# Kernel tuning notes

Hardware: AMD Instinct MI355X
Metric: run time of the kernel (lower is better)

## Reference

```python
import jax, jax.numpy as jnp
import numpy as np

N_HEAD = 8
LINEAR_DIM = 64
IN_PIXELS = 4096  # h*w = 64*64
D = N_HEAD * LINEAR_DIM  # 512
C = 128
LN_EPS = 1e-6
BN_EPS = 1e-5


def setup_inputs() -> dict:
    key = jax.random.key(0)
    ks = jax.random.split(key, 10)
    shp = (16, C, 64, 64)
    # Kaiming-uniform-ish small init for weights (torch Linear weight layout: [out, in])
    def lin(k, out_f, in_f):
        lim = 1.0 / np.sqrt(in_f)
        return jax.random.uniform(k, (out_f, in_f), jnp.float32, -lim, lim)
    return {
        "v": jax.random.normal(ks[0], shp, jnp.float32),
        "k": jax.random.normal(ks[1], shp, jnp.float32),
        "q": jax.random.normal(ks[2], shp, jnp.float32),
        "w_qs": lin(ks[3], D, IN_PIXELS),
        "w_ks": lin(ks[4], D, IN_PIXELS),
        "w_vs": lin(ks[5], D, IN_PIXELS),
        "w_fc": lin(ks[6], IN_PIXELS, D),
        "ln_gamma": jnp.ones((D,), jnp.float32),
        "ln_beta": jnp.zeros((D,), jnp.float32),
        "temperature": jnp.asarray(IN_PIXELS ** 0.5, jnp.float32),
        "bn_gamma": jnp.ones((C,), jnp.float32),
        "bn_beta": jnp.zeros((C,), jnp.float32),
    }


def _layer_norm(x, gamma, beta):
    # torch-faithful: unbiased std (ddof=1), divide by (std + eps)
    mean = jnp.mean(x, axis=-1, keepdims=True)
    var = jnp.var(x, axis=-1, keepdims=True, ddof=1)
    std = jnp.sqrt(var)
    return gamma * (x - mean) / (std + LN_EPS) + beta


def reference(v, k, q, w_qs, w_ks, w_vs, w_fc, ln_gamma, ln_beta, temperature, bn_gamma, bn_beta):
    b, c, h, w = q.shape
    P = h * w
    qf = q.reshape(b, c, P)
    kf = k.reshape(b, c, P)
    vf = v.reshape(b, c, P)
    residual = vf
    # QKV projections: [b,c,P] @ W^T -> [b,c,D] -> [b,nh,c,ld]
    def proj(x, W):
        y = jnp.einsum('bcp,dp->bcd', x, W)
        return y.reshape(b, c, N_HEAD, LINEAR_DIM).transpose(0, 2, 1, 3)
    Q = proj(qf, w_qs)
    K = proj(kf, w_ks)
    V = proj(vf, w_vs)
    # channel-wise attention: scores [b,nh,c,c]
    scores = jnp.einsum('bhcd,bhed->bhce', Q / temperature, K)
    attn = jax.nn.softmax(scores, axis=-1)
    O = jnp.einsum('bhce,bhed->bhcd', attn, V)
    O = O.transpose(0, 2, 1, 3).reshape(b, c, N_HEAD * LINEAR_DIM)
    # Swish -> LayerNorm -> fc -> residual
    O = O * jax.nn.sigmoid(O)
    O = _layer_norm(O, ln_gamma, ln_beta)
    O = jnp.einsum('bcd,pd->bcp', O, w_fc)
    out = (residual + O).reshape(b, c, h, w)
    # BatchNorm2d in training mode: batch stats over (b,h,w), biased variance
    mean = jnp.mean(out, axis=(0, 2, 3), keepdims=True)
    var = jnp.var(out, axis=(0, 2, 3), keepdims=True)
    out = (out - mean) / jnp.sqrt(var + BN_EPS)
    out = out * bn_gamma[None, :, None, None] + bn_beta[None, :, None, None]
    return out
```

## Files before the change

### kernel.cpp

```cpp
#include <hip/hip_runtime.h>
#include <hip/hip_bf16.h>
#include <stdint.h>

typedef __attribute__((ext_vector_type(8))) short bf16x8;
typedef __attribute__((ext_vector_type(4))) float f32x4;

#define AS1(p) ((const __attribute__((address_space(1))) uint32_t*)(p))
#define AS3(p) ((__attribute__((address_space(3))) uint32_t*)(p))

__device__ __forceinline__ ushort f2bf(float f) {
  uint32_t u = __float_as_uint(f);
  uint32_t r = (u + 0x7fffu + ((u >> 16) & 1u)) >> 16;
  return (ushort)r;
}

__device__ __forceinline__ uint4 cvt8u(float4 a0, float4 a1) {
  uint4 r;
  asm("v_cvt_pk_bf16_f32 %0, %1, %2" : "=v"(r.x) : "v"(a0.x), "v"(a0.y));
  asm("v_cvt_pk_bf16_f32 %0, %1, %2" : "=v"(r.y) : "v"(a0.z), "v"(a0.w));
  asm("v_cvt_pk_bf16_f32 %0, %1, %2" : "=v"(r.z) : "v"(a1.x), "v"(a1.y));
  asm("v_cvt_pk_bf16_f32 %0, %1, %2" : "=v"(r.w) : "v"(a1.z), "v"(a1.w));
  return r;
}

__global__ __launch_bounds__(256) void pack4(
    const float* __restrict__ s0, const float* __restrict__ s1,
    const float* __restrict__ s2, const float* __restrict__ s3,
    ushort* __restrict__ o0, ushort* __restrict__ o1,
    ushort* __restrict__ o2, ushort* __restrict__ o3, int n)
{
  const float* s; ushort* o;
  switch (blockIdx.y) {
    case 0: s = s0; o = o0; break;
    case 1: s = s1; o = o1; break;
    case 2: s = s2; o = o2; break;
    default: s = s3; o = o3; break;
  }
  int stride = gridDim.x * 1024;
  for (int i = (blockIdx.x * 256 + threadIdx.x) * 4; i < n; i += stride) {
    float4 v = *(const float4*)(s + i);
    ushort4 u;
    u.x = f2bf(v.x); u.y = f2bf(v.y); u.z = f2bf(v.z); u.w = f2bf(v.w);
    *(ushort4*)(o + i) = u;
  }
}

__global__ __launch_bounds__(256) void gemm_qkv(
    const float* __restrict__ aq, const float* __restrict__ ak, const float* __restrict__ av,
    const ushort* __restrict__ wq, const ushort* __restrict__ wk, const ushort* __restrict__ wv,
    float* __restrict__ part, int lgs)
{
  __shared__ __align__(16) ushort At[128 * 64];
  __shared__ __align__(16) ushort Bt[2][128 * 64];
  int per = gridDim.x >> 3;
  int bid = blockIdx.x;
  int swz = (bid & 7) * per + (bid >> 3);
  int y = swz & 3, x = (swz >> 2) & 15, zz = swz >> 6;
  int g = zz >> lgs, s = zz & ((1 << lgs) - 1);
  const float* A; const ushort* Bm;
  if (g == 0)      { A = aq; Bm = wq; }
  else if (g == 1) { A = ak; Bm = wk; }
  else             { A = av; Bm = wv; }
  float* Pd = part + ((size_t)zz) * 1048576;
  const int K = 4096;
  const int kchunk = K >> lgs;
  const int k0 = s * kchunk, kend = k0 + kchunk;
  int rowBase = x * 128;
  int colBase = y * 128;
  int tid = threadIdx.x, l = tid & 63, w = tid >> 6;
  int wr = w >> 1, wc = w & 1, fr = l & 15, fq = l >> 4;

  int arow = tid >> 3;
  int aslot = tid & 7;
  const float* Abase = A + (size_t)(rowBase + arow) * K + aslot * 8;

  f32x4 acc[4][4];
#pragma unroll
  for (int m = 0; m < 4; ++m)
#pragma unroll
    for (int n = 0; n < 4; ++n) acc[m][n] = (f32x4){0.f, 0.f, 0.f, 0.f};

  float4 areg[4][2];
  auto loadA = [&](int ktn) {
#pragma unroll
    for (int j = 0; j < 4; ++j) {
      const float* p = Abase + (size_t)(j * 32) * K + ktn;
      areg[j][0] = *(const float4*)p;
      areg[j][1] = *(const float4*)(p + 4);
    }
  };
  auto cvtWriteA = [&]() {
#pragma unroll
    for (int j = 0; j < 4; ++j) {
      int row = j * 32 + arow;
      int sw = aslot ^ (row & 7);
      *(uint4*)((char*)At + row * 128 + sw * 16) = cvt8u(areg[j][0], areg[j][1]);
    }
  };
  auto stageB = [&](ushort* Bbuf, int ktn) {
#pragma unroll
    for (int j = 0; j < 4; ++j) {
      int c = ((w * 4 + j) << 6) + l;
      int row = c >> 3, slot = c & 7;
      int srccol = (slot ^ (row & 7)) * 8;
      __builtin_amdgcn_global_load_lds(AS1(Bm + (size_t)(colBase + row) * K + ktn + srccol),
                                       AS3((char*)Bbuf + c * 16), 16, 0, 0);
    }
  };
  auto mfmaPhase = [&](const ushort* Bbuf) {
#pragma unroll
    for (int kc = 0; kc < 2; ++kc) {
      bf16x8 af[4], bv[4];
#pragma unroll
      for (int m = 0; m < 4; ++m) {
        int r = wr * 64 + m * 16 + fr;
        int sl = (kc * 4 + fq) ^ (fr & 7);
        af[m] = *(const bf16x8*)((const char*)At + r * 128 + sl * 16);
      }
#pragma unroll
      for (int n = 0; n < 4; ++n) {
        int r = wc * 64 + n * 16 + fr;
        int sl = (kc * 4 + fq) ^ (fr & 7);
        bv[n] = *(const bf16x8*)((const char*)Bbuf + r * 128 + sl * 16);
      }
#pragma unroll
      for (int m = 0; m < 4; ++m)
#pragma unroll
        for (int n = 0; n < 4; ++n)
          acc[m][n] = __builtin_amdgcn_mfma_f32_16x16x32_bf16(af[m], bv[n], acc[m][n], 0, 0, 0);
    }
  };

  loadA(k0);
  stageB(Bt[0], k0);
  cvtWriteA();
  __syncthreads();

  int buf = 0;
#pragma unroll 1
  for (int kt = k0; kt < kend; kt += 64) {
    bool more = (kt + 64) < kend;
    if (more) { loadA(kt + 64); stageB(Bt[buf ^ 1], kt + 64); }
    mfmaPhase(Bt[buf]);
    __syncthreads();
    if (more) cvtWriteA();
    __syncthreads();
    buf ^= 1;
  }

#pragma unroll
  for (int m = 0; m < 4; ++m)
#pragma unroll
    for (int n = 0; n < 4; ++n)
#pragma unroll
      for (int r = 0; r < 4; ++r) {
        int row = rowBase + wr * 64 + m * 16 + fq * 4 + r;
        int col = colBase + wc * 64 + n * 16 + fr;
        Pd[(size_t)row * 512 + col] = acc[m][n][r];
      }
}

__global__ __launch_bounds__(256) void reduce_qkv(
    const float* __restrict__ part, ushort* __restrict__ Qp, ushort* __restrict__ Kp,
    ushort* __restrict__ Vp, int lgs)
{
  int g = blockIdx.y;
  ushort* dst = g == 0 ? Qp : (g == 1 ? Kp : Vp);
  const float* p = part + (((size_t)g) << lgs) * 1048576;
  int i = (blockIdx.x * 256 + threadIdx.x) * 4;
  float4 acc = *(const float4*)(p + i);
  int splits = 1 << lgs;
  for (int s = 1; s < splits; ++s) {
    float4 b = *(const float4*)(p + (size_t)s * 1048576 + i);
    acc.x += b.x; acc.y += b.y; acc.z += b.z; acc.w += b.w;
  }
  ushort4 u;
  u.x = f2bf(acc.x); u.y = f2bf(acc.y); u.z = f2bf(acc.z); u.w = f2bf(acc.w);
  *(ushort4*)(dst + i) = u;
}

__global__ __launch_bounds__(256) void attn(
    const ushort* __restrict__ Qp, const ushort* __restrict__ Kp, const ushort* __restrict__ Vp,
    float* __restrict__ Obuf, const float* __restrict__ temp)
{
  __shared__ __align__(16) ushort Qs[64 * 64];
  __shared__ __align__(16) ushort Ks[128 * 64];
  __shared__ __align__(16) ushort Vt[64 * 128];
  __shared__ __align__(16) float  Sl[64 * 128];
  __shared__ __align__(16) ushort Pl[64 * 128];
  __shared__ float rsum[64];
  int bh = blockIdx.y, b = bh >> 3, h = bh & 7;
  int c0 = blockIdx.x * 64;
  int tid = threadIdx.x, l = tid & 63, w = tid >> 6;
  int wr = w >> 1, wc = w & 1, fr = l & 15, fq = l >> 4;
  float invT = 1.0f / temp[0];
  const size_t rowQ = (size_t)(b * 128 + c0);

#pragma unroll
  for (int j = 0; j < 2; ++j) {
    int c = ((w * 2 + j) << 6) + l, row = c >> 3, cc = c & 7;
    __builtin_amdgcn_global_load_lds(AS1(Qp + (rowQ + row) * 512 + h * 64 + cc * 8),
                                     AS3((char*)Qs + (w * 2 + j) * 1024), 16, 0, 0);
  }
#pragma unroll
  for (int j = 0; j < 4; ++j) {
    int c = ((w * 4 + j) << 6) + l, row = c >> 3, cc = c & 7;
    __builtin_amdgcn_global_load_lds(AS1(Kp + (size_t)(b * 128 + row) * 512 + h * 64 + cc * 8),
                                     AS3((char*)Ks + (w * 4 + j) * 1024), 16, 0, 0);
  }
#pragma unroll
  for (int t = 0; t < 4; ++t) {
    int ch = tid + t * 256, e = ch >> 3, d0 = (ch & 7) * 8;
    bf16x8 vv = *(const bf16x8*)(Vp + (size_t)(b * 128 + e) * 512 + h * 64 + d0);
#pragma unroll
    for (int j = 0; j < 8; ++j) Vt[(d0 + j) * 128 + e] = (ushort)vv[j];
  }
  __syncthreads();

  f32x4 sa[2][4];
#pragma unroll
  for (int m = 0; m < 2; ++m)
#pragma unroll
    for (int n = 0; n < 4; ++n) sa[m][n] = (f32x4){0.f, 0.f, 0.f, 0.f};
#pragma unroll
  for (int kc = 0; kc < 2; ++kc) {
    bf16x8 aQ[2], bK[4];
#pragma unroll
    for (int m = 0; m < 2; ++m)
      aQ[m] = *(const bf16x8*)&Qs[(wr * 32 + m * 16 + fr) * 64 + kc * 32 + fq * 8];
#pragma unroll
    for (int n = 0; n < 4; ++n)
      bK[n] = *(const bf16x8*)&Ks[(wc * 64 + n * 16 + fr) * 64 + kc * 32 + fq * 8];
#pragma unroll
    for (int m = 0; m < 2; ++m)
#pragma unroll
      for (int n = 0; n < 4; ++n)
        sa[m][n] = __builtin_amdgcn_mfma_f32_16x16x32_bf16(aQ[m], bK[n], sa[m][n], 0, 0, 0);
  }
#pragma unroll
  for (int m = 0; m < 2; ++m)
#pragma unroll
    for (int n = 0; n < 4; ++n)
#pragma unroll
      for (int r = 0; r < 4; ++r)
        Sl[(wr * 32 + m * 16 + fq * 4 + r) * 128 + wc * 64 + n * 16 + fr] = sa[m][n][r] * invT;
  __syncthreads();

  {
    int row = tid >> 2, qq = tid & 3;
    const float* srow = Sl + row * 128 + qq * 32;
    float4 va[8];
#pragma unroll
    for (int i = 0; i < 8; ++i) va[i] = *(const float4*)(srow + i * 4);
    float mx = -1e30f;
#pragma unroll
    for (int i = 0; i < 8; ++i)
      mx = fmaxf(mx, fmaxf(fmaxf(va[i].x, va[i].y), fmaxf(va[i].z, va[i].w)));
    mx = fmaxf(mx, __shfl_xor(mx, 1));
    mx = fmaxf(mx, __shfl_xor(mx, 2));
    float ssum = 0.f;
    ushort* prow = Pl + row * 128 + qq * 32;
#pragma unroll
    for (int i = 0; i < 8; ++i) {
      float e0 = __expf(va[i].x - mx), e1 = __expf(va[i].y - mx);
      float e2 = __expf(va[i].z - mx), e3 = __expf(va[i].w - mx);
      ssum += (e0 + e1) + (e2 + e3);
      ushort4 u; u.x = f2bf(e0); u.y = f2bf(e1); u.z = f2bf(e2); u.w = f2bf(e3);
      *(ushort4*)(prow + i * 4) = u;
    }
    ssum += __shfl_xor(ssum, 1);
    ssum += __shfl_xor(ssum, 2);
    if (qq == 0) rsum[row] = ssum;
  }
  __syncthreads();

  f32x4 oa[2][2];
#pragma unroll
  for (int m = 0; m < 2; ++m)
#pragma unroll
    for (int n = 0; n < 2; ++n) oa[m][n] = (f32x4){0.f, 0.f, 0.f, 0.f};
#pragma unroll
  for (int kc = 0; kc < 4; ++kc) {
    bf16x8 aP[2], bV[2];
#pragma unroll
    for (int m = 0; m < 2; ++m)
      aP[m] = *(const bf16x8*)&Pl[(wr * 32 + m * 16 + fr) * 128 + kc * 32 + fq * 8];
#pragma unroll
    for (int n = 0; n < 2; ++n)
      bV[n] = *(const bf16x8*)&Vt[(wc * 32 + n * 16 + fr) * 128 + kc * 32 + fq * 8];
#pragma unroll
    for (int m = 0; m < 2; ++m)
#pragma unroll
      for (int n = 0; n < 2; ++n)
        oa[m][n] = __builtin_amdgcn_mfma_f32_16x16x32_bf16(aP[m], bV[n], oa[m][n], 0, 0, 0);
  }
#pragma unroll
  for (int m = 0; m < 2; ++m)
#pragma unroll
    for (int n = 0; n < 2; ++n)
#pragma unroll
      for (int r = 0; r < 4; ++r) {
        int row = wr * 32 + m * 16 + fq * 4 + r, col = wc * 32 + n * 16 + fr;
        Obuf[(rowQ + row) * 512 + h * 64 + col] = oa[m][n][r] / rsum[row];
      }
}

__global__ __launch_bounds__(256) void swish_ln(
    const float* __restrict__ O, ushort* __restrict__ X,
    const float* __restrict__ gamma, const float* __restrict__ beta)
{
  int row = blockIdx.x * 4 + (threadIdx.x >> 6);
  int lane = threadIdx.x & 63;
  const float* x = O + (size_t)row * 512 + lane * 8;
  float4 va = *(const float4*)(x);
  float4 vb = *(const float4*)(x + 4);
  float y[8] = {va.x, va.y, va.z, va.w, vb.x, vb.y, vb.z, vb.w};
  float s = 0.f, sq = 0.f;
#pragma unroll
  for (int i = 0; i < 8; ++i) {
    y[i] = y[i] / (1.f + __expf(-y[i]));
    s += y[i]; sq += y[i] * y[i];
  }
#pragma unroll
  for (int o = 1; o < 64; o <<= 1) { s += __shfl_xor(s, o); sq += __shfl_xor(sq, o); }
  float mean = s * (1.f / 512.f);
  float var = (sq - s * mean) * (1.f / 511.f);
  float inv = 1.f / (sqrtf(var) + 1e-6f);
  const float4 g0 = *(const float4*)(gamma + lane * 8);
  const float4 g1 = *(const float4*)(gamma + lane * 8 + 4);
  const float4 b0 = *(const float4*)(beta + lane * 8);
  const float4 b1 = *(const float4*)(beta + lane * 8 + 4);
  float gg[8] = {g0.x, g0.y, g0.z, g0.w, g1.x, g1.y, g1.z, g1.w};
  float bb[8] = {b0.x, b0.y, b0.z, b0.w, b1.x, b1.y, b1.z, b1.w};
  ushort u[8];
#pragma unroll
  for (int i = 0; i < 8; ++i) u[i] = f2bf(gg[i] * (y[i] - mean) * inv + bb[i]);
  *(uint4*)(X + (size_t)row * 512 + lane * 8) = *(uint4*)u;
}

__global__ __launch_bounds__(256) void gemm_fc(
    const ushort* __restrict__ A, const ushort* __restrict__ Bm,
    const float* __restrict__ resid, float* __restrict__ out,
    float* __restrict__ bn_sum, float* __restrict__ bn_sq)
{
  __shared__ __align__(16) ushort At[128 * 64];
  __shared__ __align__(16) ushort Bt[128 * 64];
  __shared__ float csum[128], csq[128];
  const int K = 512;
  int rowBase = blockIdx.x * 128;
  int colBase = blockIdx.y * 128;
  int tid = threadIdx.x, l = tid & 63, w = tid >> 6;
  int wr = w >> 1, wc = w & 1, fr = l & 15, fq = l >> 4;
  if (tid < 128) { csum[tid] = 0.f; csq[tid] = 0.f; }
  f32x4 acc[4][4];
#pragma unroll
  for (int m = 0; m < 4; ++m)
#pragma unroll
    for (int n = 0; n < 4; ++n) acc[m][n] = (f32x4){0.f, 0.f, 0.f, 0.f};

  for (int kt = 0; kt < K; kt += 64) {
#pragma unroll
    for (int j = 0; j < 4; ++j) {
      int c = ((w * 4 + j) << 6) + l;
      int row = c >> 3, cc = c & 7;
      __builtin_amdgcn_global_load_lds(AS1(A + (size_t)(rowBase + row) * K + kt + cc * 8),
                                       AS3((char*)At + (w * 4 + j) * 1024), 16, 0, 0);
      __builtin_amdgcn_global_load_lds(AS1(Bm + (size_t)(colBase + row) * K + kt + cc * 8),
                                       AS3((char*)Bt + (w * 4 + j) * 1024), 16, 0, 0);
    }
    __syncthreads();
#pragma unroll
    for (int kc = 0; kc < 2; ++kc) {
      bf16x8 af[4], bfv[4];
#pragma unroll
      for (int m = 0; m < 4; ++m)
        af[m] = *(const bf16x8*)&At[(wr * 64 + m * 16 + fr) * 64 + kc * 32 + fq * 8];
#pragma unroll
      for (int n = 0; n < 4; ++n)
        bfv[n] = *(const bf16x8*)&Bt[(wc * 64 + n * 16 + fr) * 64 + kc * 32 + fq * 8];
#pragma unroll
      for (int m = 0; m < 4; ++m)
#pragma unroll
        for (int n = 0; n < 4; ++n)
          acc[m][n] = __builtin_amdgcn_mfma_f32_16x16x32_bf16(af[m], bfv[n], acc[m][n], 0, 0, 0);
    }
    __syncthreads();
  }
#pragma unroll
  for (int m = 0; m < 4; ++m)
#pragma unroll
    for (int r = 0; r < 4; ++r) {
      float ps = 0.f, pq = 0.f;
#pragma unroll
      for (int n = 0; n < 4; ++n) {
        int row = rowBase + wr * 64 + m * 16 + fq * 4 + r;
        int col = colBase + wc * 64 + n * 16 + fr;
        size_t idx = (size_t)row * 4096 + col;
        float val = acc[m][n][r] + resid[idx];
        out[idx] = val;
        ps += val; pq += val * val;
      }
#pragma unroll
      for (int o = 1; o < 16; o <<= 1) { ps += __shfl_xor(ps, o); pq += __shfl_xor(pq, o); }
      if (fr == 0) {
        int ch = wr * 64 + m * 16 + fq * 4 + r;
        atomicAdd(&csum[ch], ps);
        atomicAdd(&csq[ch], pq);
      }
    }
  __syncthreads();
  if (tid < 128) {
    atomicAdd(&bn_sum[tid], csum[tid]);
    atomicAdd(&bn_sq[tid], csq[tid]);
  }
}

__global__ __launch_bounds__(256) void bn_norm(
    float* __restrict__ out, const float* __restrict__ bn_sum, const float* __restrict__ bn_sq,
    const float* __restrict__ gamma, const float* __restrict__ beta)
{
  const float inv_n = 1.f / 65536.f;
  int stride = gridDim.x * blockDim.x;
  for (int v = blockIdx.x * blockDim.x + threadIdx.x; v < 2097152; v += stride) {
    int elem = v * 4;
    int ch = (elem >> 12) & 127;
    float mean = bn_sum[ch] * inv_n;
    float var = bn_sq[ch] * inv_n - mean * mean;
    float g = gamma[ch] * rsqrtf(var + 1e-5f);
    float bta = beta[ch];
    float4 x = *(float4*)(out + elem);
    x.x = (x.x - mean) * g + bta;
    x.y = (x.y - mean) * g + bta;
    x.z = (x.z - mean) * g + bta;
    x.w = (x.w - mean) * g + bta;
    *(float4*)(out + elem) = x;
  }
}

extern "C" void kernel_launch(void* const* d_in, const int* in_sizes, int n_in,
                              void* d_out, int out_size, void* d_ws, size_t ws_size,
                              hipStream_t stream)
{
  const float* v_in = (const float*)d_in[0];
  const float* k_in = (const float*)d_in[1];
  const float* q_in = (const float*)d_in[2];
  const float* w_qs = (const float*)d_in[3];
  const float* w_ks = (const float*)d_in[4];
  const float* w_vs = (const float*)d_in[5];
  const float* w_fc = (const float*)d_in[6];
  const float* ln_g = (const float*)d_in[7];
  const float* ln_b = (const float*)d_in[8];
  const float* temp = (const float*)d_in[9];
  const float* bn_g = (const float*)d_in[10];
  const float* bn_b = (const float*)d_in[11];
  float* out = (float*)d_out;

  char* ws = (char*)d_ws;
  size_t off = 0;
  auto alloc = [&](size_t bytes) { char* p = ws + off; off += bytes; return p; };
  ushort* wq  = (ushort*)alloc(512ull * 4096 * 2);
  ushort* wk  = (ushort*)alloc(512ull * 4096 * 2);
  ushort* wv  = (ushort*)alloc(512ull * 4096 * 2);
  ushort* wfc = (ushort*)alloc(512ull * 4096 * 2);
  ushort* Qp  = (ushort*)alloc(2048ull * 512 * 2);
  ushort* Kp  = (ushort*)alloc(2048ull * 512 * 2);
  ushort* Vp  = (ushort*)alloc(2048ull * 512 * 2);
  float*  Obuf= (float*)alloc(2048ull * 512 * 4);
  ushort* X16 = (ushort*)alloc(2048ull * 512 * 2);
  float*  bns = (float*)alloc(128 * 4);
  float*  bnq = (float*)alloc(128 * 4);

  int lgs = 2;
  if (off + (3ull << lgs) * 1048576 * 4 > ws_size) lgs = 1;
  if (off + (3ull << lgs) * 1048576 * 4 > ws_size) lgs = 0;
  float* part = (float*)alloc((3ull << lgs) * 1048576 * 4);

  hipMemsetAsync(bns, 0, 256 * 4, stream);

  pack4<<<dim3(512, 4), 256, 0, stream>>>(w_qs, w_ks, w_vs, w_fc, wq, wk, wv, wfc,
                                          512 * 4096);
  gemm_qkv<<<16 * 4 * (3 << lgs), 256, 0, stream>>>(q_in, k_in, v_in, wq, wk, wv, part, lgs);
  reduce_qkv<<<dim3(1024, 3), 256, 0, stream>>>(part, Qp, Kp, Vp, lgs);
  attn<<<dim3(2, 128), 256, 0, stream>>>(Qp, Kp, Vp, Obuf, temp);
  swish_ln<<<512, 256, 0, stream>>>(Obuf, X16, ln_g, ln_b);
  gemm_fc<<<dim3(16, 32), 256, 0, stream>>>(X16, wfc, v_in, out, bns, bnq);
  bn_norm<<<2048, 256, 0, stream>>>(out, bns, bnq, bn_g, bn_b);
}
```

Baseline: 121.6 us.

## Deepen QKV GEMM pipeline with double A registers and explicit waitcnt barriers

Restructures the QKV projection GEMM main loop into a two-step unrolled software pipeline. A tiles are prefetched two steps ahead into alternating register sets, and the __syncthreads calls are replaced by manual s_waitcnt vmcnt/lgkmcnt counters plus raw s_barrier and sched_barrier. It also sets launch_bounds occupancy to 3 blocks per SM. The goal is to hide global-load latency behind MFMA work and cut barrier overhead, at the cost of more registers and fragile hand-counted wait values that assume nsteps is even and at least 2.

```diff
diff --git a/kernel.cpp b/kernel.cpp
--- a/kernel.cpp
+++ b/kernel.cpp
@@ -7,6 +7,13 @@
 
 #define AS1(p) ((const __attribute__((address_space(1))) uint32_t*)(p))
 #define AS3(p) ((__attribute__((address_space(3))) uint32_t*)(p))
+
+#define VMCNT12 asm volatile("s_waitcnt vmcnt(12)" ::: "memory")
+#define VMCNT4  asm volatile("s_waitcnt vmcnt(4)" ::: "memory")
+#define VMCNT0  asm volatile("s_waitcnt vmcnt(0)" ::: "memory")
+#define LGKM0   asm volatile("s_waitcnt lgkmcnt(0)" ::: "memory")
+#define SBAR    __builtin_amdgcn_s_barrier()
+#define SCHED0  __builtin_amdgcn_sched_barrier(0)
 
 __device__ __forceinline__ ushort f2bf(float f) {
   uint32_t u = __float_as_uint(f);
@@ -45,7 +52,7 @@
   }
 }
 
-__global__ __launch_bounds__(256) void gemm_qkv(
+__global__ __launch_bounds__(256, 3) void gemm_qkv(
     const float* __restrict__ aq, const float* __restrict__ ak, const float* __restrict__ av,
     const ushort* __restrict__ wq, const ushort* __restrict__ wk, const ushort* __restrict__ wv,
     float* __restrict__ part, int lgs)
@@ -64,7 +71,8 @@
   float* Pd = part + ((size_t)zz) * 1048576;
   const int K = 4096;
   const int kchunk = K >> lgs;
-  const int k0 = s * kchunk, kend = k0 + kchunk;
+  const int k0 = s * kchunk;
+  const int nsteps = kchunk >> 6;
   int rowBase = x * 128;
   int colBase = y * 128;
   int tid = threadIdx.x, l = tid & 63, w = tid >> 6;
@@ -80,34 +88,39 @@
 #pragma unroll
     for (int n = 0; n < 4; ++n) acc[m][n] = (f32x4){0.f, 0.f, 0.f, 0.f};
 
-  float4 areg[4][2];
-  auto loadA = [&](int ktn) {
+  float4 regA[4][2], regB[4][2];
+
+  auto loadTo = [&](float4 (&rg)[4][2], int step) {
+    int ktn = k0 + step * 64;
 #pragma unroll
     for (int j = 0; j < 4; ++j) {
       const float* p = Abase + (size_t)(j * 32) * K + ktn;
-      areg[j][0] = *(const float4*)p;
-      areg[j][1] = *(const float4*)(p + 4);
+      rg[j][0] = *(const float4*)p;
+      rg[j][1] = *(const float4*)(p + 4);
     }
   };
-  auto cvtWriteA = [&]() {
+  auto cvtWrite = [&](float4 (&rg)[4][2]) {
 #pragma unroll
     for (int j = 0; j < 4; ++j) {
       int row = j * 32 + arow;
       int sw = aslot ^ (row & 7);
-      *(uint4*)((char*)At + row * 128 + sw * 16) = cvt8u(areg[j][0], areg[j][1]);
+      *(uint4*)((char*)At + row * 128 + sw * 16) = cvt8u(rg[j][0], rg[j][1]);
     }
   };
-  auto stageB = [&](ushort* Bbuf, int ktn) {
+  auto stageB = [&](int bufIdx, int step) {
+    int ktn = k0 + step * 64;
+    char* Bbuf = (char*)Bt[bufIdx];
 #pragma unroll
     for (int j = 0; j < 4; ++j) {
       int c = ((w * 4 + j) << 6) + l;
       int row = c >> 3, slot = c & 7;
       int srccol = (slot ^ (row & 7)) * 8;
       __builtin_amdgcn_global_load_lds(AS1(Bm + (size_t)(colBase + row) * K + ktn + srccol),
-                                       AS3((char*)Bbuf + c * 16), 16, 0, 0);
+                                       AS3(Bbuf + c * 16), 16, 0, 0);
     }
   };
-  auto mfmaPhase = [&](const ushort* Bbuf) {
+  auto mfmaPhase = [&](int bufIdx) {
+    const char* Bbuf = (const char*)Bt[bufIdx];
 #pragma unroll
     for (int kc = 0; kc < 2; ++kc) {
       bf16x8 af[4], bv[4];
@@ -121,7 +134,7 @@
       for (int n = 0; n < 4; ++n) {
         int r = wc * 64 + n * 16 + fr;
         int sl = (kc * 4 + fq) ^ (fr & 7);
-        bv[n] = *(const bf16x8*)((const char*)Bbuf + r * 128 + sl * 16);
+        bv[n] = *(const bf16x8*)(Bbuf + r * 128 + sl * 16);
       }
 #pragma unroll
       for (int m = 0; m < 4; ++m)
@@ -131,22 +144,52 @@
     }
   };
 
-  loadA(k0);
-  stageB(Bt[0], k0);
-  cvtWriteA();
-  __syncthreads();
-
-  int buf = 0;
-#pragma unroll 1
-  for (int kt = k0; kt < kend; kt += 64) {
-    bool more = (kt + 64) < kend;
-    if (more) { loadA(kt + 64); stageB(Bt[buf ^ 1], kt + 64); }
-    mfmaPhase(Bt[buf]);
-    __syncthreads();
-    if (more) cvtWriteA();
-    __syncthreads();
-    buf ^= 1;
-  }
+  loadTo(regA, 0);
+  loadTo(regB, 1);
+  stageB(0, 0);
+  VMCNT12;
+  SCHED0;
+  cvtWrite(regA);
+  LGKM0;
+
+  for (int it = 0; it < nsteps - 2; it += 2) {
+    loadTo(regA, it + 2);
+    stageB(1, it + 1);
+    VMCNT12;
+    SBAR;
+    SCHED0;
+    mfmaPhase(0);
+    LGKM0;
+    SBAR;
+    cvtWrite(regB);
+    LGKM0;
+
+    loadTo(regB, it + 3);
+    stageB(0, it + 2);
+    VMCNT12;
+    SBAR;
+    SCHED0;
+    mfmaPhase(1);
+    LGKM0;
+    SBAR;
+    cvtWrite(regA);
+    LGKM0;
+  }
+
+  stageB(1, nsteps - 1);
+  VMCNT4;
+  SBAR;
+  SCHED0;
+  mfmaPhase(0);
+  LGKM0;
+  SBAR;
+  cvtWrite(regB);
+  LGKM0;
+
+  VMCNT0;
+  SBAR;
+  SCHED0;
+  mfmaPhase(1);
 
 #pragma unroll
   for (int m = 0; m < 4; ++m)
```

Measured after the change: 232.1 us. +90.9%, slower.
